# Kernel tuning notes

Hardware: AMD Instinct MI355X
Metric: run time of the kernel (lower is better)

Reference implementation:

```python
import jax, jax.numpy as jnp
import numpy as np

N, M, D = 500000, 128, 16

def setup_inputs() -> dict:
    key = jax.random.key(0)
    k1, k2, k3 = jax.random.split(key, 3)
    points = jax.random.uniform(k1, (N, D), dtype=jnp.float32)
    centers = jax.random.uniform(k2, (M, D), dtype=jnp.float32)
    # module initializes covs_inv_sqrt = 15*I per center; add small noise so it's non-trivial
    covs_inv_sqrt = 15.0 * jnp.eye(D, dtype=jnp.float32)[None, :, :] \
        + 0.1 * jax.random.normal(k3, (M, D, D), dtype=jnp.float32)
    weights = jnp.ones((M,), dtype=jnp.float32)
    threshold = jnp.zeros((1,), dtype=jnp.float32)
    return {"points": points, "centers": centers, "covs_inv_sqrt": covs_inv_sqrt,
            "weights": weights, "threshold": threshold}

def reference(points, centers, covs_inv_sqrt, weights, threshold):
    # refresh(): covs_inv = L @ L^T per center
    covs_inv = jnp.einsum('jde,jfe->jdf', covs_inv_sqrt, covs_inv_sqrt)  # [M,D,D]
    # equal_clusters=True branch
    w = jnp.abs(weights)
    center_prs = w / (w.sum() + 1e-30)
    coefs = center_prs * jnp.sqrt(jnp.linalg.det(covs_inv))  # [M]
    # Mahalanobis quadratic form (x-c)^T S (x-c) expanded as xSx - 2 xSc + cSc
    S_flat = covs_inv.reshape(M, D * D)                          # [M,D^2]
    xx = (points[:, :, None] * points[:, None, :]).reshape(-1, D * D)  # [N,D^2]
    Sc = jnp.einsum('jde,je->jd', covs_inv, centers)             # [M,D]
    cSc = jnp.einsum('jd,jd->j', centers, Sc)                    # [M]
    q = xx @ S_flat.T - 2.0 * (points @ Sc.T) + cSc[None, :]     # [N,M]
    d_ij = -0.5 * q
    # weighted online logsumexp over centers (KeOps logsumexp with weight Vj(coefs))
    log_lik = jax.nn.logsumexp(d_ij, axis=1, b=coefs[None, :], keepdims=True)  # [N,1]
    return log_lik - threshold
```

## Files before the change

kernel.cpp:

```cpp
#include <hip/hip_runtime.h>
#include <math.h>

#define M_CTR 128
#define D_DIM 16
#define KSTEPS 10
#define NSLOT 80
#define GRID_MAIN 1024
#define WS_CONST_F32_OFF 10240

typedef _Float16 half8 __attribute__((ext_vector_type(8)));
typedef float f32x16 __attribute__((ext_vector_type(16)));

struct SlotTab { unsigned char a[NSLOT]; unsigned char b[NSLOT]; unsigned char m[NSLOT]; };
constexpr SlotTab make_tab() {
    SlotTab T{};
    int s = 0;
    for (int d = 0; d < 8; ++d) { T.a[s] = (unsigned char)d; T.b[s] = (unsigned char)d; T.m[s] = 0; ++s; }
    for (int d = 0; d < 8; ++d)
        for (int f = d + 1; f < 8; ++f) { T.a[s] = (unsigned char)d; T.b[s] = (unsigned char)f; T.m[s] = 0; ++s; }
    for (int d = 0; d < 8; ++d)
        for (int f2 = d + 1; f2 < 8; ++f2) { T.a[s] = (unsigned char)d; T.b[s] = (unsigned char)(f2 + 8); T.m[s] = 0; ++s; }
    for (int d = 0; d < 4; ++d) { T.a[s] = (unsigned char)d; T.b[s] = (unsigned char)(d + 8); T.m[s] = 1; ++s; }
    for (int d = 0; d < 8; ++d) { T.a[s] = (unsigned char)d; T.b[s] = 0; T.m[s] = 2; ++s; }
    for (; s < NSLOT; ++s) { T.a[s] = 0; T.b[s] = 0; T.m[s] = 3; }
    return T;
}
constexpr SlotTab TAB = make_tab();

__global__ __launch_bounds__(64) void gmm_prep_kernel(
    const float* __restrict__ centers,
    const float* __restrict__ Lmat,
    const float* __restrict__ weights,
    float* __restrict__ ws)
{
    const int j    = blockIdx.x;
    const int lane = threadIdx.x;
    const int r    = lane & 15;

    __shared__ float S_lds[D_DIM][D_DIM + 1];
    __shared__ float Scp_lds[D_DIM];

    float Lr[D_DIM];
    {
        const float4* Lrow = (const float4*)(Lmat + (size_t)j * 256 + r * 16);
        #pragma unroll
        for (int q = 0; q < 4; ++q) {
            const float4 v = Lrow[q];
            Lr[q * 4 + 0] = v.x; Lr[q * 4 + 1] = v.y;
            Lr[q * 4 + 2] = v.z; Lr[q * 4 + 3] = v.w;
        }
    }

    float u[D_DIM];
    #pragma unroll
    for (int e = 0; e < D_DIM; ++e) u[e] = Lr[e];
    float logdet = 0.f;
    #pragma unroll
    for (int k = 0; k < D_DIM; ++k) {
        const float pk = __shfl(u[k], k);
        logdet += logf(fabsf(pk));
        const float f = u[k] * (1.0f / pk);
        #pragma unroll
        for (int c = k + 1; c < D_DIM; ++c) {
            const float rkc = __shfl(u[c], k);
            if (r > k) u[c] -= f * rkc;
        }
    }

    #pragma unroll
    for (int f = 0; f < D_DIM; ++f) {
        float acc = 0.f;
        #pragma unroll
        for (int e = 0; e < D_DIM; ++e) acc += Lr[e] * __shfl(Lr[e], f);
        if (lane < D_DIM) S_lds[lane][f] = acc;
    }
    __syncthreads();

    float c[D_DIM];
    {
        const float4* cc = (const float4*)(centers + (size_t)j * D_DIM);
        #pragma unroll
        for (int q = 0; q < 4; ++q) {
            const float4 v = cc[q];
            c[q * 4 + 0] = v.x - 0.5f; c[q * 4 + 1] = v.y - 0.5f;
            c[q * 4 + 2] = v.z - 0.5f; c[q * 4 + 3] = v.w - 0.5f;
        }
    }
    if (lane < D_DIM) {
        float acc = 0.f;
        #pragma unroll
        for (int f = 0; f < D_DIM; ++f) acc += S_lds[lane][f] * c[f];
        Scp_lds[lane] = acc;
    }
    __syncthreads();
    float cSc = 0.f;
    #pragma unroll
    for (int d = 0; d < D_DIM; ++d) cSc += c[d] * Scp_lds[d];

    float wa = fabsf(weights[lane]) + fabsf(weights[lane + 64]);
    #pragma unroll
    for (int off = 32; off > 0; off >>= 1) wa += __shfl_xor(wa, off);
    const float lc = logf(fabsf(weights[j])) - logf(wa + 1e-30f) + logdet;

    float* constsG = ws + WS_CONST_F32_OFF;
    if (lane == 0) constsG[j] = lc - 0.5f * cSc;

    if (lane < 2 * KSTEPS) {
        const int t  = lane >> 1;
        const int hi = lane & 1;
        const int h  = j >> 6;
        const int mt = (j >> 5) & 1;
        half8 hv;
        for (int e = 0; e < 8; ++e) {
            const int s  = t * 8 + e;
            const int mm = TAB.m[s], a = TAB.a[s], b = TAB.b[s];
            float val;
            if (mm == 0) {
                const int d = hi ? ((a + 8) & 15) : a;
                const int f = hi ? ((b + 8) & 15) : b;
                val = (d == f) ? -0.5f * S_lds[d][d] : -S_lds[d][f];
            } else if (mm == 1) {
                const int d = a + 4 * hi, f = a + 8 + 4 * hi;
                val = -S_lds[d][f];
            } else if (mm == 2) {
                val = Scp_lds[a + 8 * hi];
            } else {
                val = 0.f;
            }
            hv[e] = (_Float16)val;
        }
        char* dst = (char*)ws + ((((h * 2 + mt) * KSTEPS + t) * 64) + hi * 32 + (j & 31)) * 16;
        *(half8*)dst = hv;
    }
}

__global__ __launch_bounds__(128, 2) void gmm_main_kernel(
    const float* __restrict__ points,
    const float* __restrict__ wsf,
    const float* __restrict__ thr,
    float* __restrict__ out,
    int ntiles)
{
    const int tid = threadIdx.x;
    const int w   = tid >> 6;
    const int l   = tid & 63;
    const int col = l & 31;
    const bool hi = (l >> 5) != 0;

    half8 A[2][KSTEPS];
    {
        const char* wsb = (const char*)wsf;
        #pragma unroll
        for (int mt = 0; mt < 2; ++mt)
            #pragma unroll
            for (int t = 0; t < KSTEPS; ++t)
                A[mt][t] = *(const half8*)(wsb + ((((w * 2 + mt) * KSTEPS + t) * 64) + l) * 16);
    }

    float cst[32];
    {
        const float* cstG = wsf + WS_CONST_F32_OFF;
        #pragma unroll
        for (int mt = 0; mt < 2; ++mt)
            #pragma unroll
            for (int rr = 0; rr < 16; ++rr)
                cst[mt * 16 + rr] =
                    cstG[w * 64 + mt * 32 + (rr & 3) + 8 * (rr >> 2) + 4 * (l >> 5)];
    }

    const float thrv = thr[0];
    __shared__ float lm[2][32], ls[2][32];

    for (int tile = blockIdx.x; tile < ntiles; tile += GRID_MAIN) {
        float z[D_DIM];
        {
            const float4* px = (const float4*)(points + ((size_t)tile * 32 + col) * D_DIM);
            #pragma unroll
            for (int q = 0; q < 4; ++q) {
                const float4 v = px[q];
                z[q * 4 + 0] = v.x - 0.5f; z[q * 4 + 1] = v.y - 0.5f;
                z[q * 4 + 2] = v.z - 0.5f; z[q * 4 + 3] = v.w - 0.5f;
            }
        }
        float zs8[16], z4l[4], z4h[4];
        #pragma unroll
        for (int i = 0; i < 16; ++i) zs8[i] = hi ? z[(i + 8) & 15] : z[i];
        #pragma unroll
        for (int i = 0; i < 4; ++i) {
            z4l[i] = hi ? z[i + 4]  : z[i];
            z4h[i] = hi ? z[i + 12] : z[i + 8];
        }

        f32x16 acc0 = {0.f, 0.f, 0.f, 0.f, 0.f, 0.f, 0.f, 0.f,
                       0.f, 0.f, 0.f, 0.f, 0.f, 0.f, 0.f, 0.f};
        f32x16 acc1 = acc0;

        #pragma unroll
        for (int t = 0; t < KSTEPS; ++t) {
            half8 bf;
            #pragma unroll
            for (int e = 0; e < 8; ++e) {
                const int s  = t * 8 + e;
                const int mm = TAB.m[s], a = TAB.a[s], b = TAB.b[s];
                float p = (mm == 0) ? zs8[a] * zs8[b]
                        : (mm == 1) ? z4l[a] * z4h[a]
                        : (mm == 2) ? zs8[a]
                        : 0.f;
                bf[e] = (_Float16)p;
            }
            acc0 = __builtin_amdgcn_mfma_f32_32x32x16_f16(A[0][t], bf, acc0, 0, 0, 0);
            acc1 = __builtin_amdgcn_mfma_f32_32x32x16_f16(A[1][t], bf, acc1, 0, 0, 0);
        }

        float v[32];
        #pragma unroll
        for (int rr = 0; rr < 16; ++rr) {
            v[rr]      = acc0[rr] + cst[rr];
            v[16 + rr] = acc1[rr] + cst[16 + rr];
        }
        float tm[16];
        #pragma unroll
        for (int i = 0; i < 16; ++i) tm[i] = fmaxf(v[i], v[i + 16]);
        #pragma unroll
        for (int st = 8; st >= 1; st >>= 1)
            #pragma unroll
            for (int i = 0; i < st; ++i) tm[i] = fmaxf(tm[i], tm[i + st]);
        const float mx = tm[0];

        float s0 = 0.f, s1 = 0.f, s2 = 0.f, s3 = 0.f;
        #pragma unroll
        for (int i = 0; i < 32; i += 4) {
            s0 += __expf(v[i + 0] - mx);
            s1 += __expf(v[i + 1] - mx);
            s2 += __expf(v[i + 2] - mx);
            s3 += __expf(v[i + 3] - mx);
        }
        float ss = (s0 + s1) + (s2 + s3);

        const float om = __shfl_xor(mx, 32);
        const float os = __shfl_xor(ss, 32);
        const float M2 = fmaxf(mx, om);
        const float S2 = ss * __expf(mx - M2) + os * __expf(om - M2);

        if (l < 32) { lm[w][l] = M2; ls[w][l] = S2; }
        __syncthreads();
        if (w == 0 && l < 32) {
            const float m0 = lm[0][l], m1 = lm[1][l];
            const float MM = fmaxf(m0, m1);
            const float SS = ls[0][l] * __expf(m0 - MM) + ls[1][l] * __expf(m1 - MM);
            out[tile * 32 + l] = MM + __logf(SS) - thrv;
        }
        __syncthreads();
    }
}

extern "C" void kernel_launch(void* const* d_in, const int* in_sizes, int n_in,
                              void* d_out, int out_size, void* d_ws, size_t ws_size,
                              hipStream_t stream) {
    const float* points  = (const float*)d_in[0];
    const float* centers = (const float*)d_in[1];
    const float* covs    = (const float*)d_in[2];
    const float* weights = (const float*)d_in[3];
    const float* thr     = (const float*)d_in[4];
    float* out = (float*)d_out;
    float* ws  = (float*)d_ws;

    const int n      = in_sizes[0] / D_DIM;
    const int ntiles = n / 32;

    gmm_prep_kernel<<<M_CTR, 64, 0, stream>>>(centers, covs, weights, ws);
    gmm_main_kernel<<<GRID_MAIN, 128, 0, stream>>>(points, ws, thr, out, ntiles);
}
```

Baseline: 49.45 us.

## Prefetch next point tile, use base-2 exp in logsumexp, raise grid and occupancy

The next tile's point data is loaded right after the MFMA loop, so the load overlaps the reduction tail. The log2(e) factor is folded into the precomputed A matrices and constants, which lets the softmax use raw exp2 and log2 instructions with a single ln2 multiply at the end. The grid grows from 1024 to 4096 blocks and launch bounds ask for 4 blocks per SM, which limits registers. The added register pressure from prefetching, together with the tighter register limit, risks spills of the held A fragments. Scaling values by log2(e) before the fp16 cast also slightly shifts rounding.

```diff
diff --git a/kernel.cpp b/kernel.cpp
--- a/kernel.cpp
+++ b/kernel.cpp
@@ -5,8 +5,10 @@
 #define D_DIM 16
 #define KSTEPS 10
 #define NSLOT 80
-#define GRID_MAIN 1024
+#define GRID_MAIN 4096
 #define WS_CONST_F32_OFF 10240
+#define LOG2E 1.4426950408889634f
+#define LN2   0.6931471805599453f
 
 typedef _Float16 half8 __attribute__((ext_vector_type(8)));
 typedef float f32x16 __attribute__((ext_vector_type(16)));
@@ -103,7 +105,7 @@
     const float lc = logf(fabsf(weights[j])) - logf(wa + 1e-30f) + logdet;
 
     float* constsG = ws + WS_CONST_F32_OFF;
-    if (lane == 0) constsG[j] = lc - 0.5f * cSc;
+    if (lane == 0) constsG[j] = (lc - 0.5f * cSc) * LOG2E;
 
     if (lane < 2 * KSTEPS) {
         const int t  = lane >> 1;
@@ -127,14 +129,14 @@
             } else {
                 val = 0.f;
             }
-            hv[e] = (_Float16)val;
+            hv[e] = (_Float16)(val * LOG2E);
         }
         char* dst = (char*)ws + ((((h * 2 + mt) * KSTEPS + t) * 64) + hi * 32 + (j & 31)) * 16;
         *(half8*)dst = hv;
     }
 }
 
-__global__ __launch_bounds__(128, 2) void gmm_main_kernel(
+__global__ __launch_bounds__(128, 4) void gmm_main_kernel(
     const float* __restrict__ points,
     const float* __restrict__ wsf,
     const float* __restrict__ thr,
@@ -171,17 +173,21 @@
     const float thrv = thr[0];
     __shared__ float lm[2][32], ls[2][32];
 
-    for (int tile = blockIdx.x; tile < ntiles; tile += GRID_MAIN) {
+    const float4* pbase = (const float4*)points;
+    int tile = blockIdx.x;
+    float4 pf0, pf1, pf2, pf3;
+    if (tile < ntiles) {
+        const float4* px = pbase + ((size_t)tile * 32 + col) * 4;
+        pf0 = px[0]; pf1 = px[1]; pf2 = px[2]; pf3 = px[3];
+    }
+
+    for (; tile < ntiles; tile += GRID_MAIN) {
         float z[D_DIM];
-        {
-            const float4* px = (const float4*)(points + ((size_t)tile * 32 + col) * D_DIM);
-            #pragma unroll
-            for (int q = 0; q < 4; ++q) {
-                const float4 v = px[q];
-                z[q * 4 + 0] = v.x - 0.5f; z[q * 4 + 1] = v.y - 0.5f;
-                z[q * 4 + 2] = v.z - 0.5f; z[q * 4 + 3] = v.w - 0.5f;
-            }
-        }
+        z[0]=pf0.x-0.5f; z[1]=pf0.y-0.5f; z[2]=pf0.z-0.5f; z[3]=pf0.w-0.5f;
+        z[4]=pf1.x-0.5f; z[5]=pf1.y-0.5f; z[6]=pf1.z-0.5f; z[7]=pf1.w-0.5f;
+        z[8]=pf2.x-0.5f; z[9]=pf2.y-0.5f; z[10]=pf2.z-0.5f; z[11]=pf2.w-0.5f;
+        z[12]=pf3.x-0.5f; z[13]=pf3.y-0.5f; z[14]=pf3.z-0.5f; z[15]=pf3.w-0.5f;
+
         float zs8[16], z4l[4], z4h[4];
         #pragma unroll
         for (int i = 0; i < 16; ++i) zs8[i] = hi ? z[(i + 8) & 15] : z[i];
@@ -212,6 +218,14 @@
             acc1 = __builtin_amdgcn_mfma_f32_32x32x16_f16(A[1][t], bf, acc1, 0, 0, 0);
         }
 
+        {
+            const int nxt = tile + GRID_MAIN;
+            if (nxt < ntiles) {
+                const float4* px = pbase + ((size_t)nxt * 32 + col) * 4;
+                pf0 = px[0]; pf1 = px[1]; pf2 = px[2]; pf3 = px[3];
+            }
+        }
+
         float v[32];
         #pragma unroll
         for (int rr = 0; rr < 16; ++rr) {
@@ -221,34 +235,39 @@
         float tm[16];
         #pragma unroll
         for (int i = 0; i < 16; ++i) tm[i] = fmaxf(v[i], v[i + 16]);
-        #pragma unroll
-        for (int st = 8; st >= 1; st >>= 1)
-            #pragma unroll
-            for (int i = 0; i < st; ++i) tm[i] = fmaxf(tm[i], tm[i + st]);
-        const float mx = tm[0];
+        float r0 = fmaxf(fmaxf(tm[0], tm[1]), tm[2]);
+        float r1 = fmaxf(fmaxf(tm[3], tm[4]), tm[5]);
+        float r2 = fmaxf(fmaxf(tm[6], tm[7]), tm[8]);
+        float r3 = fmaxf(fmaxf(tm[9], tm[10]), tm[11]);
+        float r4 = fmaxf(fmaxf(tm[12], tm[13]), tm[14]);
+        float ra = fmaxf(fmaxf(r0, r1), r2);
+        float rb = fmaxf(fmaxf(r3, r4), tm[15]);
+        const float mx = fmaxf(ra, rb);
 
         float s0 = 0.f, s1 = 0.f, s2 = 0.f, s3 = 0.f;
         #pragma unroll
         for (int i = 0; i < 32; i += 4) {
-            s0 += __expf(v[i + 0] - mx);
-            s1 += __expf(v[i + 1] - mx);
-            s2 += __expf(v[i + 2] - mx);
-            s3 += __expf(v[i + 3] - mx);
+            s0 += __builtin_amdgcn_exp2f(v[i + 0] - mx);
+            s1 += __builtin_amdgcn_exp2f(v[i + 1] - mx);
+            s2 += __builtin_amdgcn_exp2f(v[i + 2] - mx);
+            s3 += __builtin_amdgcn_exp2f(v[i + 3] - mx);
         }
         float ss = (s0 + s1) + (s2 + s3);
 
         const float om = __shfl_xor(mx, 32);
         const float os = __shfl_xor(ss, 32);
         const float M2 = fmaxf(mx, om);
-        const float S2 = ss * __expf(mx - M2) + os * __expf(om - M2);
+        const float S2 = ss * __builtin_amdgcn_exp2f(mx - M2)
+                       + os * __builtin_amdgcn_exp2f(om - M2);
 
         if (l < 32) { lm[w][l] = M2; ls[w][l] = S2; }
         __syncthreads();
         if (w == 0 && l < 32) {
             const float m0 = lm[0][l], m1 = lm[1][l];
             const float MM = fmaxf(m0, m1);
-            const float SS = ls[0][l] * __expf(m0 - MM) + ls[1][l] * __expf(m1 - MM);
-            out[tile * 32 + l] = MM + __logf(SS) - thrv;
+            const float SS = ls[0][l] * __builtin_amdgcn_exp2f(m0 - MM)
+                           + ls[1][l] * __builtin_amdgcn_exp2f(m1 - MM);
+            out[tile * 32 + l] = fmaf(LN2, MM + __builtin_amdgcn_logf(SS), -thrv);
         }
         __syncthreads();
     }
```

Result: slower. 143.5 us (+190.2%).
